# Kernel tuning notes

Measured on AMD Instinct MI355X. Metric: run time of the kernel, lower is better.

Reference implementation:

```python
import jax, jax.numpy as jnp
import numpy as np

N = 50000
E = 800000
IN_C = 128
HID = 16
HEADS = 8
OUT_C = 128
NEG_SLOPE = 0.2
EPS = 1e-16


def setup_inputs() -> dict:
    key = jax.random.key(0)
    ks = jax.random.split(key, 12)
    x = jax.random.normal(ks[0], (N, IN_C), dtype=jnp.float32)
    edge_index = jax.random.randint(ks[1], (2, E), 0, N, dtype=jnp.int32)
    s1 = 1.0 / np.sqrt(IN_C)
    s2 = 1.0 / np.sqrt(HID * HEADS)
    W1 = jax.random.normal(ks[2], (IN_C, HEADS * HID), dtype=jnp.float32) * s1
    att_src1 = jax.random.normal(ks[3], (HEADS, HID), dtype=jnp.float32) * s1
    att_dst1 = jax.random.normal(ks[4], (HEADS, HID), dtype=jnp.float32) * s1
    b1 = jnp.zeros((HEADS * HID,), dtype=jnp.float32)
    W2 = jax.random.normal(ks[5], (HEADS * HID, OUT_C), dtype=jnp.float32) * s2
    att_src2 = jax.random.normal(ks[6], (1, OUT_C), dtype=jnp.float32) * s2
    att_dst2 = jax.random.normal(ks[7], (1, OUT_C), dtype=jnp.float32) * s2
    b2 = jnp.zeros((OUT_C,), dtype=jnp.float32)
    return {"x": x, "edge_index": edge_index, "W1": W1, "att_src1": att_src1,
            "att_dst1": att_dst1, "b1": b1, "W2": W2, "att_src2": att_src2,
            "att_dst2": att_dst2, "b2": b2}


def _add_self_loops(edge_index, n):
    loop = jnp.arange(n, dtype=edge_index.dtype)
    src = jnp.concatenate([edge_index[0], loop])
    dst = jnp.concatenate([edge_index[1], loop])
    return src, dst


def gat_conv(x, src, dst, W, att_src, att_dst, bias, heads, out_c, concat):
    n = x.shape[0]
    h = (x @ W).reshape(n, heads, out_c)          # [N, H, C]
    a_src = jnp.einsum('nhc,hc->nh', h, att_src)  # [N, H]
    a_dst = jnp.einsum('nhc,hc->nh', h, att_dst)
    e = a_src[src] + a_dst[dst]                   # [E', H]
    e = jax.nn.leaky_relu(e, NEG_SLOPE)
    # segment softmax over edges grouped by destination node
    m = jax.ops.segment_max(e, dst, num_segments=n)          # [N, H]
    m = jnp.where(jnp.isfinite(m), m, 0.0)
    ex = jnp.exp(e - m[dst])                                  # [E', H]
    denom = jax.ops.segment_sum(ex, dst, num_segments=n)      # [N, H]
    alpha = ex / (denom[dst] + EPS)                            # [E', H]
    msg = alpha[:, :, None] * h[src]                           # [E', H, C]
    out = jax.ops.segment_sum(msg, dst, num_segments=n)       # [N, H, C]
    if concat:
        out = out.reshape(n, heads * out_c)
    else:
        out = out.mean(axis=1)
    return out + bias


def reference(x, edge_index, W1, att_src1, att_dst1, b1, W2, att_src2, att_dst2, b2):
    src, dst = _add_self_loops(edge_index, N)
    h = gat_conv(x, src, dst, W1, att_src1, att_dst1, b1, HEADS, HID, True)
    h = jax.nn.relu(h)
    # dropout is identity in eval mode
    out = gat_conv(h, src, dst, W2, att_src2, att_dst2, b2, 1, OUT_C, False)
    return out
```

## Files before the change

kernel.cpp:

```cpp
#include <hip/hip_runtime.h>


constexpr int N_NODES = 50000;
constexpr int E_EDGES = 800000;
constexpr int ETOT = E_EDGES + N_NODES;
constexpr float NEG_SLOPE = 0.2f;
constexpr float EPS = 1e-16f;
constexpr int SCAN_BLK = 512;
constexpr int NBLK_SCAN = (N_NODES + SCAN_BLK - 1) / SCAN_BLK;

typedef short bf16x8 __attribute__((ext_vector_type(8)));
typedef float f32x4 __attribute__((ext_vector_type(4)));

__device__ __forceinline__ float lrelu(float x) { return x > 0.f ? x : NEG_SLOPE * x; }
__device__ __forceinline__ ushort f2bf(float f) {
    uint u = __float_as_uint(f);
    return (ushort)((u + 0x7fffu + ((u >> 16) & 1u)) >> 16);
}
__device__ __forceinline__ float bf2f(uint u) { return __uint_as_float(u << 16); }

__device__ __forceinline__ void fma8(float* acc, uint4 p, float w, float& ws) {
    ws += w;
    acc[0] += w * bf2f(p.x & 0xffffu); acc[1] += w * bf2f(p.x >> 16);
    acc[2] += w * bf2f(p.y & 0xffffu); acc[3] += w * bf2f(p.y >> 16);
    acc[4] += w * bf2f(p.z & 0xffffu); acc[5] += w * bf2f(p.z >> 16);
    acc[6] += w * bf2f(p.w & 0xffffu); acc[7] += w * bf2f(p.w >> 16);
}

__global__ __launch_bounds__(256) void convert_W(const float* __restrict__ W1,
                                                 const float* __restrict__ W2,
                                                 const float* __restrict__ attS2,
                                                 const float* __restrict__ attD2,
                                                 ushort* __restrict__ W1t,
                                                 ushort* __restrict__ W2t,
                                                 float* __restrict__ vs,
                                                 float* __restrict__ vd,
                                                 uint* __restrict__ cnt) {
    const int t = threadIdx.x;
    if (blockIdx.x >= 2) {
        const int i = (blockIdx.x - 2) * 256 + t;
        if (i < N_NODES) cnt[i] = 0;
        return;
    }
    const float* W = (blockIdx.x == 0) ? W1 : W2;
    ushort* Wt = (blockIdx.x == 0) ? W1t : W2t;
    const int n = t >> 1, k0 = (t & 1) * 64;
    for (int k = 0; k < 64; k += 2) {
        uint lo = f2bf(W[(size_t)(k0 + k) * 128 + n]);
        uint hi = f2bf(W[(size_t)(k0 + k + 1) * 128 + n]);
        *(uint*)&Wt[(size_t)n * 128 + k0 + k] = lo | (hi << 16);
    }
    if (blockIdx.x == 1) {
        const int k = t & 127;
        const float* av = (t < 128) ? attS2 : attD2;
        float* dst = (t < 128) ? vs : vd;
        float s = 0.f;
        for (int c = 0; c < 128; ++c) s += W2[(size_t)k * 128 + c] * av[c];
        dst[k] = s;
    }
}

__global__ __launch_bounds__(256) void count_rank(const int* __restrict__ ei,
                                                  uint* __restrict__ cnt,
                                                  ushort* __restrict__ rank) {
    int e = blockIdx.x * blockDim.x + threadIdx.x;
    if (e >= ETOT) return;
    int d = (e < E_EDGES) ? ei[E_EDGES + e] : (e - E_EDGES);
    uint old = atomicAdd(&cnt[d], 1u);
    rank[e] = (ushort)old;
}

__global__ __launch_bounds__(SCAN_BLK) void block_sums(const uint* __restrict__ cnt,
                                                       int* __restrict__ bsum) {
    __shared__ int sm[SCAN_BLK];
    int i = blockIdx.x * SCAN_BLK + threadIdx.x;
    sm[threadIdx.x] = (i < N_NODES) ? (int)cnt[i] : 0;
    __syncthreads();
    for (int off = SCAN_BLK / 2; off > 0; off >>= 1) {
        if (threadIdx.x < off) sm[threadIdx.x] += sm[threadIdx.x + off];
        __syncthreads();
    }
    if (threadIdx.x == 0) bsum[blockIdx.x] = sm[0];
}

__global__ __launch_bounds__(SCAN_BLK) void scan_final_fused(const uint* __restrict__ cnt,
                                                             const int* __restrict__ bsum,
                                                             int* __restrict__ rowptr) {
    __shared__ int sb[128];
    __shared__ int sm[SCAN_BLK];
    const int t = threadIdx.x;
    if (t < 128) sb[t] = (t < NBLK_SCAN) ? bsum[t] : 0;
    __syncthreads();
    for (int off = 1; off < 128; off <<= 1) {
        int v = 0;
        if (t < 128 && t >= off) v = sb[t - off];
        __syncthreads();
        if (t < 128) sb[t] += v;
        __syncthreads();
    }
    const int bid = blockIdx.x;
    const int bpre = sb[bid] - bsum[bid];

    const int i = bid * SCAN_BLK + t;
    const int v = (i < N_NODES) ? (int)cnt[i] : 0;
    sm[t] = v;
    __syncthreads();
    for (int off = 1; off < SCAN_BLK; off <<= 1) {
        int x = (t >= off) ? sm[t - off] : 0;
        __syncthreads();
        sm[t] += x;
        __syncthreads();
    }
    if (i < N_NODES) rowptr[i] = bpre + sm[t] - v;
    if (bid == 0 && t == 0) rowptr[N_NODES] = ETOT;
}

__global__ __launch_bounds__(256) void scatter_kernel(const int* __restrict__ ei,
                                                      const int* __restrict__ rowptr,
                                                      const ushort* __restrict__ rank,
                                                      ushort* __restrict__ csrc) {
    int e = blockIdx.x * blockDim.x + threadIdx.x;
    if (e >= ETOT) return;
    int s, d;
    if (e < E_EDGES) { s = ei[e]; d = ei[E_EDGES + e]; }
    else             { s = d = e - E_EDGES; }
    const int pos = rowptr[d] + (int)rank[e];
    __builtin_nontemporal_store((ushort)s, &csrc[pos]);
}

template <bool BF16IN, bool ATT8, bool ATTIN>
__global__ __launch_bounds__(256) void mfma_gemm(const void* __restrict__ Xv,
                                                 const ushort* __restrict__ Wt,
                                                 ushort* __restrict__ H,
                                                 const float* __restrict__ attS,
                                                 const float* __restrict__ attD,
                                                 float* __restrict__ aS,
                                                 float* __restrict__ aD,
                                                 int nrows) {
    __shared__ __align__(16) char smem[16384 + 32768];
    ushort* lx = (ushort*)smem;
    ushort* lw = (ushort*)(smem + 16384);
    float*  hs = (float*)smem;

    const int t = threadIdx.x;
    const int r0 = blockIdx.x * 64;

    {
        const int n = t >> 1, half = t & 1;
        const ushort* src = Wt + (size_t)n * 128 + half * 64;
        #pragma unroll
        for (int c = 0; c < 8; ++c) {
            int cx = half * 8 + c;
            uint4 v = *(const uint4*)(src + c * 8);
            *(uint4*)&lw[(n * 16 + (cx ^ (n & 7))) * 8] = v;
        }
    }
    {
        const int r = t >> 2, q = t & 3;
        const int grow = r0 + r;
        const uint4 z = {0, 0, 0, 0};
        #pragma unroll
        for (int cc = 0; cc < 4; ++cc) {
            int cx = q * 4 + cc;
            uint4 packed = z;
            if (grow < nrows) {
                if (BF16IN) {
                    packed = *(const uint4*)((const ushort*)Xv + (size_t)grow * 128 + cx * 8);
                } else {
                    const float* X = (const float*)Xv;
                    const float4 f0 = *(const float4*)(X + (size_t)grow * 128 + cx * 8);
                    const float4 f1 = *(const float4*)(X + (size_t)grow * 128 + cx * 8 + 4);
                    packed.x = (uint)f2bf(f0.x) | ((uint)f2bf(f0.y) << 16);
                    packed.y = (uint)f2bf(f0.z) | ((uint)f2bf(f0.w) << 16);
                    packed.z = (uint)f2bf(f1.x) | ((uint)f2bf(f1.y) << 16);
                    packed.w = (uint)f2bf(f1.z) | ((uint)f2bf(f1.w) << 16);
                }
            }
            *(uint4*)&lx[(r * 16 + (cx ^ (r & 7))) * 8] = packed;
        }
    }
    __syncthreads();

    const int wv = t >> 6, l = t & 63;
    const int row = wv * 16 + (l & 15);
    const int lg = l >> 4;
    f32x4 acc[8] = {};

    #pragma unroll
    for (int kb = 0; kb < 4; ++kb) {
        const int cx = kb * 4 + lg;
        bf16x8 a = *(const bf16x8*)&lx[(row * 16 + (cx ^ (row & 7))) * 8];
        #pragma unroll
        for (int nt = 0; nt < 8; ++nt) {
            const int n = nt * 16 + (l & 15);
            bf16x8 b = *(const bf16x8*)&lw[(n * 16 + (cx ^ (n & 7))) * 8];
            acc[nt] = __builtin_amdgcn_mfma_f32_16x16x32_bf16(a, b, acc[nt], 0, 0, 0);
        }
    }

    #pragma unroll
    for (int reg = 0; reg < 4; ++reg) {
        const int grow = r0 + wv * 16 + lg * 4 + reg;
        if (grow < nrows) {
            #pragma unroll
            for (int nt = 0; nt < 8; ++nt)
                H[(size_t)grow * 128 + nt * 16 + (l & 15)] = f2bf(acc[nt][reg]);
        }
    }

    if (ATT8) {
        __syncthreads();
        #pragma unroll
        for (int reg = 0; reg < 4; ++reg) {
            const int r = wv * 16 + lg * 4 + reg;
            #pragma unroll
            for (int nt = 0; nt < 8; ++nt)
                hs[r * 130 + nt * 16 + (l & 15)] = acc[nt][reg];
        }
        __syncthreads();
        for (int q = t; q < 512; q += 256) {
            const int r = q >> 3, h = q & 7;
            if (r0 + r < nrows) {
                float sv = 0.f, dv = 0.f;
                #pragma unroll
                for (int j = 0; j < 16; ++j) {
                    const float hv = hs[r * 130 + h * 16 + j];
                    sv += hv * attS[h * 16 + j];
                    dv += hv * attD[h * 16 + j];
                }
                aS[(size_t)(r0 + r) * 8 + h] = sv;
                aD[(size_t)(r0 + r) * 8 + h] = dv;
            }
        }
    }

    if (ATTIN) {
        const int r = t >> 2, qq = t & 3;
        float ps = 0.f, pd = 0.f;
        #pragma unroll
        for (int cc = 0; cc < 4; ++cc) {
            const int cx = qq * 4 + cc;
            const uint4 p = *(const uint4*)&lx[(r * 16 + (cx ^ (r & 7))) * 8];
            const uint w[4] = {p.x, p.y, p.z, p.w};
            #pragma unroll
            for (int q = 0; q < 4; ++q) {
                const float e0 = bf2f(w[q] & 0xffffu);
                const float e1 = bf2f(w[q] >> 16);
                ps += e0 * attS[cx * 8 + 2 * q] + e1 * attS[cx * 8 + 2 * q + 1];
                pd += e0 * attD[cx * 8 + 2 * q] + e1 * attD[cx * 8 + 2 * q + 1];
            }
        }
        ps += __shfl_xor(ps, 1); ps += __shfl_xor(ps, 2);
        pd += __shfl_xor(pd, 1); pd += __shfl_xor(pd, 2);
        if (qq == 0 && r0 + r < nrows) { aS[r0 + r] = ps; aD[r0 + r] = pd; }
    }
}

__global__ __launch_bounds__(256) void agg8(const int* __restrict__ rowptr,
                                            const ushort* __restrict__ csrc,
                                            const float* __restrict__ aS,
                                            const float* __restrict__ aD,
                                            const ushort* __restrict__ Hm,
                                            const float* __restrict__ bias,
                                            ushort* __restrict__ o1bf) {
    __shared__ float wlds[4][512];
    const int wv = threadIdx.x >> 6;
    const int lane = threadIdx.x & 63;
    const int g = lane >> 4, i = lane & 15, hc = i >> 1;
    const int hw = lane & 7;
    const int wid = blockIdx.x * 4 + wv;
    const int nw = gridDim.x * 4;
    const uint4 zero4 = {0, 0, 0, 0};

    for (int d = wid; d < N_NODES; d += nw) {
        const float adh = aD[(size_t)d * 8 + hw];
        const int base = rowptr[d], end = rowptr[d + 1];
        float acc[8] = {0.f, 0.f, 0.f, 0.f, 0.f, 0.f, 0.f, 0.f};
        float ws = 0.f;

        for (int c0 = base; c0 < end; c0 += 64) {
            const int rem = min(64, end - c0);
            const int s_l = (lane < rem) ? (int)csrc[c0 + lane] : 0;

            const int nwc = (rem + 7) >> 3;
            for (int jj = 0; jj < nwc; ++jj) {
                const int j = jj * 8 + (lane >> 3);
                const int sj = __shfl(s_l, j & 63);
                float w = 0.f;
                if (j < rem) w = __expf(lrelu(aS[(size_t)sj * 8 + hw] + adh));
                wlds[wv][j * 8 + hw] = w;
            }

            const int niter = (rem + 3) >> 2;
            int j = g;
            int scur = __shfl(s_l, j);
            uint4 pcur = zero4;
            if (j < rem) pcur = *(const uint4*)(Hm + (size_t)scur * 128 + i * 8);
            for (int tt = 0; tt < niter; ++tt) {
                const int jn = j + 4;
                const int snxt = __shfl(s_l, jn & 63);
                uint4 pnxt = zero4;
                if (jn < rem) pnxt = *(const uint4*)(Hm + (size_t)snxt * 128 + i * 8);
                float w = 0.f;
                if (j < rem) w = wlds[wv][j * 8 + hc];
                fma8(acc, pcur, w, ws);
                pcur = pnxt;
                j = jn;
            }
        }

        #pragma unroll
        for (int k = 0; k < 8; ++k) {
            acc[k] += __shfl_xor(acc[k], 16);
            acc[k] += __shfl_xor(acc[k], 32);
        }
        ws += __shfl_xor(ws, 16);
        ws += __shfl_xor(ws, 32);

        if (g == 0) {
            const float inv = 1.f / (ws + EPS);
            float v[8];
            #pragma unroll
            for (int k = 0; k < 8; ++k) v[k] = fmaxf(acc[k] * inv + bias[i * 8 + k], 0.f);
            uint4 pk;
            pk.x = (uint)f2bf(v[0]) | ((uint)f2bf(v[1]) << 16);
            pk.y = (uint)f2bf(v[2]) | ((uint)f2bf(v[3]) << 16);
            pk.z = (uint)f2bf(v[4]) | ((uint)f2bf(v[5]) << 16);
            pk.w = (uint)f2bf(v[6]) | ((uint)f2bf(v[7]) << 16);
            *(uint4*)(o1bf + (size_t)d * 128 + i * 8) = pk;
        }
    }
}

__global__ __launch_bounds__(256) void agg1(const int* __restrict__ rowptr,
                                            const ushort* __restrict__ csrc,
                                            const float* __restrict__ aS,
                                            const float* __restrict__ aD,
                                            const ushort* __restrict__ Hm,
                                            const float* __restrict__ bias,
                                            float* __restrict__ out) {
    const int wv = threadIdx.x >> 6;
    const int lane = threadIdx.x & 63;
    const int g = lane >> 4, i = lane & 15;
    const int wid = blockIdx.x * 4 + wv;
    const int nw = gridDim.x * 4;
    const uint4 zero4 = {0, 0, 0, 0};

    for (int d = wid; d < N_NODES; d += nw) {
        const float ad = aD[d];
        const int base = rowptr[d], end = rowptr[d + 1];
        float acc[8] = {0.f, 0.f, 0.f, 0.f, 0.f, 0.f, 0.f, 0.f};
        float ws = 0.f;

        for (int c0 = base; c0 < end; c0 += 64) {
            const int rem = min(64, end - c0);
            const int s_l = (lane < rem) ? (int)csrc[c0 + lane] : 0;
            const float w_l = (lane < rem) ? __expf(lrelu(aS[s_l] + ad)) : 0.f;

            const int niter = (rem + 3) >> 2;
            int j = g;
            int scur = __shfl(s_l, j);
            float wcur = __shfl(w_l, j);
            uint4 pcur = zero4;
            if (j < rem) pcur = *(const uint4*)(Hm + (size_t)scur * 128 + i * 8);
            for (int tt = 0; tt < niter; ++tt) {
                const int jn = j + 4;
                const int snxt = __shfl(s_l, jn & 63);
                const float wnxt = __shfl(w_l, jn & 63);
                uint4 pnxt = zero4;
                if (jn < rem) pnxt = *(const uint4*)(Hm + (size_t)snxt * 128 + i * 8);
                float w = (j < rem) ? wcur : 0.f;
                fma8(acc, pcur, w, ws);
                pcur = pnxt;
                wcur = wnxt;
                j = jn;
            }
        }

        #pragma unroll
        for (int k = 0; k < 8; ++k) {
            acc[k] += __shfl_xor(acc[k], 16);
            acc[k] += __shfl_xor(acc[k], 32);
        }
        ws += __shfl_xor(ws, 16);
        ws += __shfl_xor(ws, 32);

        if (g == 0) {
            const float inv = 1.f / (ws + EPS);
            float4 o0, o1v;
            o0.x = acc[0] * inv + bias[i * 8 + 0];
            o0.y = acc[1] * inv + bias[i * 8 + 1];
            o0.z = acc[2] * inv + bias[i * 8 + 2];
            o0.w = acc[3] * inv + bias[i * 8 + 3];
            o1v.x = acc[4] * inv + bias[i * 8 + 4];
            o1v.y = acc[5] * inv + bias[i * 8 + 5];
            o1v.z = acc[6] * inv + bias[i * 8 + 6];
            o1v.w = acc[7] * inv + bias[i * 8 + 7];
            *(float4*)(out + (size_t)d * 128 + i * 8) = o0;
            *(float4*)(out + (size_t)d * 128 + i * 8 + 4) = o1v;
        }
    }
}

extern "C" void kernel_launch(void* const* d_in, const int* in_sizes, int n_in,
                              void* d_out, int out_size, void* d_ws, size_t ws_size,
                              hipStream_t stream) {
    const float* x        = (const float*)d_in[0];
    const int*   ei       = (const int*)  d_in[1];
    const float* W1       = (const float*)d_in[2];
    const float* att_src1 = (const float*)d_in[3];
    const float* att_dst1 = (const float*)d_in[4];
    const float* b1       = (const float*)d_in[5];
    const float* W2       = (const float*)d_in[6];
    const float* att_src2 = (const float*)d_in[7];
    const float* att_dst2 = (const float*)d_in[8];
    const float* b2       = (const float*)d_in[9];
    float* out = (float*)d_out;

    ushort* Hbf  = (ushort*)d_ws;
    ushort* o1bf = Hbf + (size_t)N_NODES * 128;
    float*  aS1  = (float*)(o1bf + (size_t)N_NODES * 128);
    float*  aD1  = aS1 + (size_t)N_NODES * 8;
    float*  aS2  = aD1 + (size_t)N_NODES * 8;
    float*  aD2  = aS2 + N_NODES;
    float*  vs   = aD2 + N_NODES;
    float*  vd   = vs + 128;
    ushort* W1t  = (ushort*)(vd + 128);
    ushort* W2t  = W1t + 128 * 128;
    uint* cnt    = (uint*)(W2t + 128 * 128);
    int* rowptr  = (int*)(cnt + N_NODES + 1);
    int* bsum    = rowptr + N_NODES + 1;
    ushort* rank = (ushort*)(bsum + 128);
    ushort* csrc = rank + ETOT + 2;

    const int zblk = (N_NODES + 255) / 256;
    const int eblk = (ETOT + 255) / 256;
    const int gemm_blocks = (N_NODES + 63) / 64;
    const int agg_blocks = 2048;

    convert_W<<<2 + zblk, 256, 0, stream>>>(W1, W2, att_src2, att_dst2,
                                            W1t, W2t, vs, vd, cnt);
    count_rank<<<eblk, 256, 0, stream>>>(ei, cnt, rank);
    block_sums<<<NBLK_SCAN, SCAN_BLK, 0, stream>>>(cnt, bsum);
    scan_final_fused<<<NBLK_SCAN, SCAN_BLK, 0, stream>>>(cnt, bsum, rowptr);
    scatter_kernel<<<eblk, 256, 0, stream>>>(ei, rowptr, rank, csrc);

    mfma_gemm<false, true, false><<<gemm_blocks, 256, 0, stream>>>(
        x, W1t, Hbf, att_src1, att_dst1, aS1, aD1, N_NODES);
    agg8<<<agg_blocks, 256, 0, stream>>>(rowptr, csrc, aS1, aD1, Hbf, b1, o1bf);

    mfma_gemm<true, false, true><<<gemm_blocks, 256, 0, stream>>>(
        o1bf, W2t, Hbf, vs, vd, aS2, aD2, N_NODES);
    agg1<<<agg_blocks, 256, 0, stream>>>(rowptr, csrc, aS2, aD2, Hbf, b2, out);
}
```

Before: 198.8 us.

## Fuse CSR build into one cooperative kernel and balance aggregation by edge count

Replaces the five CSR-construction launches (weight conversion, count/rank, block sums, scan, scatter) with one cooperative kernel that separates its phases with grid.sync(), so fewer launches are needed. It also computes a per-wave start-node table so each aggregation wave handles a contiguous range of destinations with roughly equal edge counts, instead of a strided node assignment. Grid-wide barriers on 1024 blocks add sync cost and require all blocks to be co-resident. Contiguous ranges can improve locality but may leave waves imbalanced when a single node has a very high degree.

```diff
diff --git a/kernel.cpp b/kernel.cpp
--- a/kernel.cpp
+++ b/kernel.cpp
@@ -1,4 +1,7 @@
 #include <hip/hip_runtime.h>
+#include <hip/hip_cooperative_groups.h>
+
+namespace cg = cooperative_groups;
 
 
 constexpr int N_NODES = 50000;
@@ -6,8 +9,9 @@
 constexpr int ETOT = E_EDGES + N_NODES;
 constexpr float NEG_SLOPE = 0.2f;
 constexpr float EPS = 1e-16f;
-constexpr int SCAN_BLK = 512;
-constexpr int NBLK_SCAN = (N_NODES + SCAN_BLK - 1) / SCAN_BLK;
+constexpr int COOP_BLOCKS = 1024;
+constexpr int AGG_BLOCKS = 2048;
+constexpr int NW_AGG = AGG_BLOCKS * 4;
 
 typedef short bf16x8 __attribute__((ext_vector_type(8)));
 typedef float f32x4 __attribute__((ext_vector_type(4)));
@@ -27,105 +31,108 @@
     acc[6] += w * bf2f(p.w & 0xffffu); acc[7] += w * bf2f(p.w >> 16);
 }
 
-__global__ __launch_bounds__(256) void convert_W(const float* __restrict__ W1,
-                                                 const float* __restrict__ W2,
-                                                 const float* __restrict__ attS2,
-                                                 const float* __restrict__ attD2,
-                                                 ushort* __restrict__ W1t,
-                                                 ushort* __restrict__ W2t,
-                                                 float* __restrict__ vs,
-                                                 float* __restrict__ vd,
-                                                 uint* __restrict__ cnt) {
+__global__ __launch_bounds__(256) void csr_build(
+    const int* __restrict__ ei,
+    const float* __restrict__ W1, const float* __restrict__ W2,
+    const float* __restrict__ attS2, const float* __restrict__ attD2,
+    ushort* __restrict__ W1t, ushort* __restrict__ W2t,
+    float* __restrict__ vs, float* __restrict__ vd,
+    uint* __restrict__ cnt, ushort* __restrict__ rank,
+    int* __restrict__ bsum, int* __restrict__ rowptr,
+    ushort* __restrict__ csrc, int* __restrict__ wstart)
+{
+    __shared__ int sm[256];
+    __shared__ int sb[256];
+    cg::grid_group grid = cg::this_grid();
     const int t = threadIdx.x;
-    if (blockIdx.x >= 2) {
-        const int i = (blockIdx.x - 2) * 256 + t;
-        if (i < N_NODES) cnt[i] = 0;
-        return;
-    }
-    const float* W = (blockIdx.x == 0) ? W1 : W2;
-    ushort* Wt = (blockIdx.x == 0) ? W1t : W2t;
-    const int n = t >> 1, k0 = (t & 1) * 64;
-    for (int k = 0; k < 64; k += 2) {
-        uint lo = f2bf(W[(size_t)(k0 + k) * 128 + n]);
-        uint hi = f2bf(W[(size_t)(k0 + k + 1) * 128 + n]);
-        *(uint*)&Wt[(size_t)n * 128 + k0 + k] = lo | (hi << 16);
-    }
-    if (blockIdx.x == 1) {
+    const int b = blockIdx.x;
+    const int gtid = b * 256 + t;
+    const int nthr = COOP_BLOCKS * 256;
+    const int NCH = (N_NODES + 255) / 256;
+
+    if (b < 2) {
+        const float* W = (b == 0) ? W1 : W2;
+        ushort* Wt = (b == 0) ? W1t : W2t;
+        const int n = t >> 1, k0 = (t & 1) * 64;
+        for (int k = 0; k < 64; k += 2) {
+            uint lo = f2bf(W[(size_t)(k0 + k) * 128 + n]);
+            uint hi = f2bf(W[(size_t)(k0 + k + 1) * 128 + n]);
+            *(uint*)&Wt[(size_t)n * 128 + k0 + k] = lo | (hi << 16);
+        }
+    } else if (b == 2) {
         const int k = t & 127;
         const float* av = (t < 128) ? attS2 : attD2;
         float* dst = (t < 128) ? vs : vd;
         float s = 0.f;
         for (int c = 0; c < 128; ++c) s += W2[(size_t)k * 128 + c] * av[c];
         dst[k] = s;
-    }
-}
-
-__global__ __launch_bounds__(256) void count_rank(const int* __restrict__ ei,
-                                                  uint* __restrict__ cnt,
-                                                  ushort* __restrict__ rank) {
-    int e = blockIdx.x * blockDim.x + threadIdx.x;
-    if (e >= ETOT) return;
-    int d = (e < E_EDGES) ? ei[E_EDGES + e] : (e - E_EDGES);
-    uint old = atomicAdd(&cnt[d], 1u);
-    rank[e] = (ushort)old;
-}
-
-__global__ __launch_bounds__(SCAN_BLK) void block_sums(const uint* __restrict__ cnt,
-                                                       int* __restrict__ bsum) {
-    __shared__ int sm[SCAN_BLK];
-    int i = blockIdx.x * SCAN_BLK + threadIdx.x;
-    sm[threadIdx.x] = (i < N_NODES) ? (int)cnt[i] : 0;
-    __syncthreads();
-    for (int off = SCAN_BLK / 2; off > 0; off >>= 1) {
-        if (threadIdx.x < off) sm[threadIdx.x] += sm[threadIdx.x + off];
+    } else {
+        const int i = (b - 3) * 256 + t;
+        if (i < N_NODES) cnt[i] = 0;
+    }
+    grid.sync();
+
+    for (int e = gtid; e < ETOT; e += nthr) {
+        const int d = (e < E_EDGES) ? ei[E_EDGES + e] : (e - E_EDGES);
+        const uint old = atomicAdd(&cnt[d], 1u);
+        rank[e] = (ushort)old;
+    }
+    grid.sync();
+
+    if (b < NCH) {
+        const int i = b * 256 + t;
+        sm[t] = (i < N_NODES) ? (int)cnt[i] : 0;
         __syncthreads();
-    }
-    if (threadIdx.x == 0) bsum[blockIdx.x] = sm[0];
-}
-
-__global__ __launch_bounds__(SCAN_BLK) void scan_final_fused(const uint* __restrict__ cnt,
-                                                             const int* __restrict__ bsum,
-                                                             int* __restrict__ rowptr) {
-    __shared__ int sb[128];
-    __shared__ int sm[SCAN_BLK];
-    const int t = threadIdx.x;
-    if (t < 128) sb[t] = (t < NBLK_SCAN) ? bsum[t] : 0;
-    __syncthreads();
-    for (int off = 1; off < 128; off <<= 1) {
-        int v = 0;
-        if (t < 128 && t >= off) v = sb[t - off];
+        for (int off = 128; off > 0; off >>= 1) {
+            if (t < off) sm[t] += sm[t + off];
+            __syncthreads();
+        }
+        if (t == 0) bsum[b] = sm[0];
+    }
+    grid.sync();
+
+    if (b < NCH) {
+        sb[t] = (t < NCH) ? bsum[t] : 0;
         __syncthreads();
-        if (t < 128) sb[t] += v;
+        for (int off = 1; off < 256; off <<= 1) {
+            const int v = (t >= off) ? sb[t - off] : 0;
+            __syncthreads();
+            sb[t] += v;
+            __syncthreads();
+        }
+        const int bpre = sb[b] - bsum[b];
+        const int i = b * 256 + t;
+        const int v = (i < N_NODES) ? (int)cnt[i] : 0;
+        sm[t] = v;
         __syncthreads();
-    }
-    const int bid = blockIdx.x;
-    const int bpre = sb[bid] - bsum[bid];
-
-    const int i = bid * SCAN_BLK + t;
-    const int v = (i < N_NODES) ? (int)cnt[i] : 0;
-    sm[t] = v;
-    __syncthreads();
-    for (int off = 1; off < SCAN_BLK; off <<= 1) {
-        int x = (t >= off) ? sm[t - off] : 0;
-        __syncthreads();
-        sm[t] += x;
-        __syncthreads();
-    }
-    if (i < N_NODES) rowptr[i] = bpre + sm[t] - v;
-    if (bid == 0 && t == 0) rowptr[N_NODES] = ETOT;
-}
-
-__global__ __launch_bounds__(256) void scatter_kernel(const int* __restrict__ ei,
-                                                      const int* __restrict__ rowptr,
-                                                      const ushort* __restrict__ rank,
-                                                      ushort* __restrict__ csrc) {
-    int e = blockIdx.x * blockDim.x + threadIdx.x;
-    if (e >= ETOT) return;
-    int s, d;
-    if (e < E_EDGES) { s = ei[e]; d = ei[E_EDGES + e]; }
-    else             { s = d = e - E_EDGES; }
-    const int pos = rowptr[d] + (int)rank[e];
-    __builtin_nontemporal_store((ushort)s, &csrc[pos]);
+        for (int off = 1; off < 256; off <<= 1) {
+            const int x = (t >= off) ? sm[t - off] : 0;
+            __syncthreads();
+            sm[t] += x;
+            __syncthreads();
+        }
+        if (i < N_NODES) rowptr[i] = bpre + sm[t] - v;
+        if (b == 0 && t == 0) rowptr[N_NODES] = ETOT;
+    }
+    grid.sync();
+
+    for (int e = gtid; e < ETOT; e += nthr) {
+        int s, d;
+        if (e < E_EDGES) { s = ei[e]; d = ei[E_EDGES + e]; }
+        else             { s = d = e - E_EDGES; }
+        const int pos = rowptr[d] + (int)rank[e];
+        __builtin_nontemporal_store((ushort)s, &csrc[pos]);
+    }
+    for (int d = gtid; d < N_NODES; d += nthr) {
+        const long long wd = ((long long)rowptr[d] * NW_AGG) / ETOT;
+        const long long wp = (d == 0) ? -1
+                           : ((long long)rowptr[d - 1] * NW_AGG) / ETOT;
+        for (long long w = wp + 1; w <= wd; ++w) wstart[w] = d;
+    }
+    if (gtid == 0) {
+        const long long wl = ((long long)rowptr[N_NODES - 1] * NW_AGG) / ETOT;
+        for (long long w = wl + 1; w <= NW_AGG; ++w) wstart[w] = N_NODES;
+    }
 }
 
 template <bool BF16IN, bool ATT8, bool ATTIN>
@@ -257,6 +264,7 @@
 }
 
 __global__ __launch_bounds__(256) void agg8(const int* __restrict__ rowptr,
+                                            const int* __restrict__ wstart,
                                             const ushort* __restrict__ csrc,
                                             const float* __restrict__ aS,
                                             const float* __restrict__ aD,
@@ -269,10 +277,10 @@
     const int g = lane >> 4, i = lane & 15, hc = i >> 1;
     const int hw = lane & 7;
     const int wid = blockIdx.x * 4 + wv;
-    const int nw = gridDim.x * 4;
+    const int dlo = wstart[wid], dhi = wstart[wid + 1];
     const uint4 zero4 = {0, 0, 0, 0};
 
-    for (int d = wid; d < N_NODES; d += nw) {
+    for (int d = dlo; d < dhi; ++d) {
         const float adh = aD[(size_t)d * 8 + hw];
         const int base = rowptr[d], end = rowptr[d + 1];
         float acc[8] = {0.f, 0.f, 0.f, 0.f, 0.f, 0.f, 0.f, 0.f};
@@ -333,6 +341,7 @@
 }
 
 __global__ __launch_bounds__(256) void agg1(const int* __restrict__ rowptr,
+                                            const int* __restrict__ wstart,
                                             const ushort* __restrict__ csrc,
                                             const float* __restrict__ aS,
                                             const float* __restrict__ aD,
@@ -343,10 +352,10 @@
     const int lane = threadIdx.x & 63;
     const int g = lane >> 4, i = lane & 15;
     const int wid = blockIdx.x * 4 + wv;
-    const int nw = gridDim.x * 4;
+    const int dlo = wstart[wid], dhi = wstart[wid + 1];
     const uint4 zero4 = {0, 0, 0, 0};
 
-    for (int d = wid; d < N_NODES; d += nw) {
+    for (int d = dlo; d < dhi; ++d) {
         const float ad = aD[d];
         const int base = rowptr[d], end = rowptr[d + 1];
         float acc[8] = {0.f, 0.f, 0.f, 0.f, 0.f, 0.f, 0.f, 0.f};
@@ -430,26 +439,27 @@
     uint* cnt    = (uint*)(W2t + 128 * 128);
     int* rowptr  = (int*)(cnt + N_NODES + 1);
     int* bsum    = rowptr + N_NODES + 1;
-    ushort* rank = (ushort*)(bsum + 128);
+    int* wstart  = bsum + 256;
+    ushort* rank = (ushort*)(wstart + NW_AGG + 2);
     ushort* csrc = rank + ETOT + 2;
 
-    const int zblk = (N_NODES + 255) / 256;
-    const int eblk = (ETOT + 255) / 256;
     const int gemm_blocks = (N_NODES + 63) / 64;
-    const int agg_blocks = 2048;
-
-    convert_W<<<2 + zblk, 256, 0, stream>>>(W1, W2, att_src2, att_dst2,
-                                            W1t, W2t, vs, vd, cnt);
-    count_rank<<<eblk, 256, 0, stream>>>(ei, cnt, rank);
-    block_sums<<<NBLK_SCAN, SCAN_BLK, 0, stream>>>(cnt, bsum);
-    scan_final_fused<<<NBLK_SCAN, SCAN_BLK, 0, stream>>>(cnt, bsum, rowptr);
-    scatter_kernel<<<eblk, 256, 0, stream>>>(ei, rowptr, rank, csrc);
+
+    {
+        void* args[] = {(void*)&ei, (void*)&W1, (void*)&W2,
+                        (void*)&att_src2, (void*)&att_dst2,
+                        (void*)&W1t, (void*)&W2t, (void*)&vs, (void*)&vd,
+                        (void*)&cnt, (void*)&rank, (void*)&bsum,
+                        (void*)&rowptr, (void*)&csrc, (void*)&wstart};
+        hipLaunchCooperativeKernel((void*)csr_build, dim3(COOP_BLOCKS), dim3(256),
+                                   args, 0, stream);
+    }
 
     mfma_gemm<false, true, false><<<gemm_blocks, 256, 0, stream>>>(
         x, W1t, Hbf, att_src1, att_dst1, aS1, aD1, N_NODES);
-    agg8<<<agg_blocks, 256, 0, stream>>>(rowptr, csrc, aS1, aD1, Hbf, b1, o1bf);
+    agg8<<<AGG_BLOCKS, 256, 0, stream>>>(rowptr, wstart, csrc, aS1, aD1, Hbf, b1, o1bf);
 
     mfma_gemm<true, false, true><<<gemm_blocks, 256, 0, stream>>>(
         o1bf, W2t, Hbf, vs, vd, aS2, aD2, N_NODES);
-    agg1<<<agg_blocks, 256, 0, stream>>>(rowptr, csrc, aS2, aD2, Hbf, b2, out);
-}
+    agg1<<<AGG_BLOCKS, 256, 0, stream>>>(rowptr, wstart, csrc, aS2, aD2, Hbf, b2, out);
+}
```

New measurement: 569.2 us. 186% more time.
